# Optimization experiments

Measured on AMD Instinct MI355X. Metric: run time of the kernel, lower is better.

Reference implementation:

```python
import jax, jax.numpy as jnp
import numpy as np

V_TH = 1.0

def spike_fn(x):
    # Heaviside spike (surrogate gradient only matters for bwd)
    return (x > 0).astype(x.dtype)

def setup_inputs() -> dict:
    key = jax.random.key(0)
    ks = jax.random.split(key, 7)
    B, T, I = 256, 512, 512
    H, NB, O = 1024, 4, 128
    HB = H // NB
    x = jax.random.normal(ks[0], (B, T, I), dtype=jnp.float32)
    v0 = jax.random.uniform(ks[1], (B, H), dtype=jnp.float32)  # torch.rand init
    W_branch = jax.random.normal(ks[2], (NB, I, HB), dtype=jnp.float32) * (1.0 / np.sqrt(I))
    tau_n = jax.random.uniform(ks[3], (NB, HB), minval=2.0, maxval=6.0, dtype=jnp.float32)
    tau_m = jax.random.uniform(ks[4], (H,), minval=0.0, maxval=4.0, dtype=jnp.float32)
    W_out = jax.random.normal(ks[5], (H, O), dtype=jnp.float32) * (1.0 / np.sqrt(H))
    b_out = jnp.zeros((O,), dtype=jnp.float32)
    return {"x": x, "v0": v0, "W_branch": W_branch, "tau_n": tau_n,
            "tau_m": tau_m, "W_out": W_out, "b_out": b_out}

def reference(x, v0, W_branch, tau_n, tau_m, W_out, b_out):
    B, T, I = x.shape
    NB, _, HB = W_branch.shape
    H = NB * HB
    beta = jax.nn.sigmoid(tau_n)[:, None, :]   # (NB, 1, HB)
    alpha = jax.nn.sigmoid(tau_m)              # (H,)
    xt = jnp.transpose(x, (1, 0, 2))           # (T, B, I)
    mask = (jnp.arange(T) >= T // 2).astype(x.dtype)  # integrate 2nd half only

    def step(carry, inp):
        d, v, s, acc = carry
        x_t, m = inp
        branch_in = jnp.einsum('bi,nio->nbo', x_t, W_branch)  # (NB, B, HB)
        d = beta * d + (1.0 - beta) * branch_in
        total = jnp.transpose(d, (1, 0, 2)).reshape(B, H)      # cat branches dim=1
        v = alpha * v + (1.0 - alpha) * total - V_TH * s
        s = spike_fn(v - V_TH)
        acc = acc + s * m
        return (d, v, s, acc), None

    d0 = jnp.zeros((NB, B, HB), dtype=x.dtype)
    s0 = jnp.zeros((B, H), dtype=x.dtype)
    acc0 = jnp.zeros((B, H), dtype=x.dtype)
    (d, v, s, acc), _ = jax.lax.scan(step, (d0, v0, s0, acc0), (xt, mask))
    return acc @ W_out + b_out
```

## Files before the change

kernel.cpp:

```cpp
#include <hip/hip_runtime.h>
#include <hip/hip_bf16.h>

#define BSZ 256
#define TT  512
#define II  512
#define HH  1024
#define OO  128
#define BH  262144
#define TC  256

typedef short bfrag8 __attribute__((ext_vector_type(8)));
typedef float f32x4  __attribute__((ext_vector_type(4)));

__device__ __forceinline__ unsigned short f2bf(float f) {
    union { float f; unsigned int u; } c; c.f = f;
    unsigned int u = c.u;
    unsigned int r = u + 0x7fffu + ((u >> 16) & 1u);
    return (unsigned short)(r >> 16);
}
__device__ __forceinline__ float bf2f(unsigned short h) {
    union { unsigned int u; float f; } c; c.u = ((unsigned int)h) << 16;
    return c.f;
}

__device__ __forceinline__ void pack2(float f0, float f1, int& hi, int& lo) {
    __hip_bfloat162 h2 = __float22bfloat162_rn(make_float2(f0, f1));
    float r0 = f0 - __bfloat162float(h2.x);
    float r1 = f1 - __bfloat162float(h2.y);
    __hip_bfloat162 l2 = __float22bfloat162_rn(make_float2(r0, r1));
    union { __hip_bfloat162 b; int i; } ch, cl;
    ch.b = h2; cl.b = l2;
    hi = ch.i; lo = cl.i;
}

__global__ __launch_bounds__(256) void setup_k(const float* __restrict__ Wb,
                                               const float* __restrict__ v0,
                                               unsigned short* __restrict__ Whi,
                                               unsigned short* __restrict__ Wlo,
                                               float* __restrict__ dS, float* __restrict__ vS,
                                               float* __restrict__ sS, float* __restrict__ aS) {
    int idx = blockIdx.x * 256 + threadIdx.x;
    int n = idx >> 17;
    int rem = idx & 131071;
    int i = rem >> 8;
    int o = rem & 255;
    int h = (n << 8) + o;
    float w = Wb[idx];
    unsigned short hi = f2bf(w);
    float fh = bf2f(hi);
    unsigned short lo = f2bf(w - fh);
    Whi[(size_t)h * II + i] = hi;
    Wlo[(size_t)h * II + i] = lo;
    if (idx < BH) {
        dS[idx] = 0.0f; vS[idx] = v0[idx]; sS[idx] = 0.0f; aS[idx] = 0.0f;
    }
}

__global__ __launch_bounds__(256) void split_x(const float* __restrict__ X,
    unsigned short* __restrict__ Xhi, unsigned short* __restrict__ Xlo)
{
    size_t idx = ((size_t)blockIdx.x * 256 + threadIdx.x) << 3;
    f32x4 v0 = *(const f32x4*)(X + idx);
    f32x4 v1 = *(const f32x4*)(X + idx + 4);
    union { uint4 v; int i[4]; } H, L;
    pack2(v0.x, v0.y, H.i[0], L.i[0]);
    pack2(v0.z, v0.w, H.i[1], L.i[1]);
    pack2(v1.x, v1.y, H.i[2], L.i[2]);
    pack2(v1.z, v1.w, H.i[3], L.i[3]);
    *(uint4*)(Xhi + idx) = H.v;
    *(uint4*)(Xlo + idx) = L.v;
}

#define GLL16(G, Lp) __builtin_amdgcn_global_load_lds(                         \
    (const __attribute__((address_space(1))) void*)(G),                        \
    (__attribute__((address_space(3))) void*)(Lp), 16, 0, 0)

#define BAR() do { asm volatile("" ::: "memory");                              \
                   __builtin_amdgcn_s_barrier();                               \
                   asm volatile("" ::: "memory"); } while (0)

#define STAGE(K0, BUFB) do {                                                   \
    _Pragma("unroll") for (int j_ = 0; j_ < 4; ++j_) {                         \
        int w8_ = (j_ << 3) + wv;                                              \
        GLL16(gA + (K0) + ((size_t)w8_ << 12), smem + (BUFB) + (w8_ << 10));   \
        GLL16(gB + (K0) + ((size_t)w8_ << 12), smem + (BUFB) + 32768 + (w8_ << 10)); \
    } } while (0)

#define LDA2(F, BUFB, H0, L0, H1, L1) do {                                     \
    const char* p_ = smem + (BUFB) + aRow + ((F) << 11);                       \
    H0 = *(const bfrag8*)(p_ + sH);                                            \
    L0 = *(const bfrag8*)(p_ + sL);                                            \
    H1 = *(const bfrag8*)(p_ + 2048 + sH);                                     \
    L1 = *(const bfrag8*)(p_ + 2048 + sL);                                     \
} while (0)

#define LOADB(BUFB) do {                                                       \
    const char* p_ = smem + (BUFB) + bRow;                                     \
    _Pragma("unroll") for (int g_ = 0; g_ < 4; ++g_) {                         \
        bh[g_] = *(const bfrag8*)(p_ + (g_ << 11) + sH);                       \
        bl[g_] = *(const bfrag8*)(p_ + (g_ << 11) + sL);                       \
    } } while (0)

#define MFMA3(AH, AL, BHG, BLG, C) do {                                        \
    C = __builtin_amdgcn_mfma_f32_16x16x32_bf16(AH, BHG, C, 0, 0, 0);          \
    C = __builtin_amdgcn_mfma_f32_16x16x32_bf16(AH, BLG, C, 0, 0, 0);          \
    C = __builtin_amdgcn_mfma_f32_16x16x32_bf16(AL, BHG, C, 0, 0, 0);          \
} while (0)

#define MM2(F, H0, L0, H1, L1) do {                                            \
    __builtin_amdgcn_s_setprio(1);                                             \
    _Pragma("unroll") for (int g_ = 0; g_ < 4; ++g_) {                         \
        MFMA3(H0, L0, bh[g_], bl[g_], acc[F][g_]);                             \
        MFMA3(H1, L1, bh[g_], bl[g_], acc[(F) + 1][g_]);                       \
    }                                                                          \
    __builtin_amdgcn_s_setprio(0);                                             \
} while (0)

__global__ __launch_bounds__(512, 2) void gemm8(
    const unsigned short* __restrict__ Xhi, const unsigned short* __restrict__ Xlo,
    const unsigned short* __restrict__ Whi, const unsigned short* __restrict__ Wlo,
    float* __restrict__ U, int xrow0)
{
    extern __shared__ char smem[];

    const int P = blockIdx.x;
    const int L = ((P & 7) << 7) | (P >> 3);
    const int m0 = (L >> 2) << 8;
    const int h0 = (L & 3) << 8;

    const int tid = threadIdx.x;
    const int lane = tid & 63;
    const int wv = tid >> 6;
    const int l16 = lane & 15;
    const int q = lane >> 4;
    const int wm = wv >> 2, wn = wv & 3;

    const int e = l16 & 7;
    const int sH = ((q ^ e) << 4);
    const int sL = (((q + 4) ^ e) << 4);
    const int aRow = ((wm << 7) + l16) << 7;
    const int bRow = (((wn << 6) + l16) << 7) + 32768;

    const int rl = lane >> 3;
    const int sp = (lane & 7) ^ rl;
    const int grow0 = (m0 << 1) + xrow0;
    const unsigned short* gA = (sp < 4)
        ? (Xhi + ((size_t)(grow0 + rl) << 9) + (sp << 3))
        : (Xlo + ((size_t)(grow0 + rl) << 9) + ((sp - 4) << 3));
    const unsigned short* gB = (sp < 4)
        ? (Whi + ((size_t)(h0 + rl) << 9) + (sp << 3))
        : (Wlo + ((size_t)(h0 + rl) << 9) + ((sp - 4) << 3));

    f32x4 acc[8][4];
#pragma unroll
    for (int i = 0; i < 8; ++i)
#pragma unroll
        for (int j = 0; j < 4; ++j)
#pragma unroll
            for (int r = 0; r < 4; ++r) acc[i][j][r] = 0.0f;

    bfrag8 a0h, a0l, a1h, a1l;
    bfrag8 b0h, b0l, b1h, b1l;
    bfrag8 bh[4], bl[4];

    STAGE(0, 0);
    STAGE(32, 65536);
    asm volatile("s_waitcnt vmcnt(8)" ::: "memory");
    __builtin_amdgcn_s_barrier();
    asm volatile("" ::: "memory");
    LDA2(0, 0, a0h, a0l, a1h, a1l);

#pragma unroll 1
    for (int tt = 0; tt < 16; tt += 2) {
        const int k2 = (tt << 5) + 64;
        LOADB(0);
        LDA2(2, 0, b0h, b0l, b1h, b1l);
        MM2(0, a0h, a0l, a1h, a1l);
        BAR();
        LDA2(4, 0, a0h, a0l, a1h, a1l);
        MM2(2, b0h, b0l, b1h, b1l);
        BAR();
        LDA2(6, 0, b0h, b0l, b1h, b1l);
        MM2(4, a0h, a0l, a1h, a1l);
        asm volatile("s_waitcnt lgkmcnt(0)" ::: "memory");
        BAR();
        if (tt < 14) {
            STAGE(k2, 0);
            MM2(6, b0h, b0l, b1h, b1l);
            asm volatile("s_waitcnt vmcnt(8)" ::: "memory");
        } else {
            MM2(6, b0h, b0l, b1h, b1l);
            asm volatile("s_waitcnt vmcnt(0)" ::: "memory");
        }
        LDA2(0, 65536, a0h, a0l, a1h, a1l);
        BAR();
        LOADB(65536);
        LDA2(2, 65536, b0h, b0l, b1h, b1l);
        MM2(0, a0h, a0l, a1h, a1l);
        BAR();
        LDA2(4, 65536, a0h, a0l, a1h, a1l);
        MM2(2, b0h, b0l, b1h, b1l);
        BAR();
        LDA2(6, 65536, b0h, b0l, b1h, b1l);
        MM2(4, a0h, a0l, a1h, a1l);
        asm volatile("s_waitcnt lgkmcnt(0)" ::: "memory");
        BAR();
        if (tt < 13) {
            STAGE(k2 + 32, 65536);
            MM2(6, b0h, b0l, b1h, b1l);
            asm volatile("s_waitcnt vmcnt(8)" ::: "memory");
            LDA2(0, 0, a0h, a0l, a1h, a1l);
        } else {
            MM2(6, b0h, b0l, b1h, b1l);
        }
        BAR();
    }

#pragma unroll
    for (int f = 0; f < 8; ++f) {
        const int rb = m0 + (wm << 7) + (f << 4) + (q << 2);
#pragma unroll
        for (int rr = 0; rr < 4; ++rr) {
            const int m = rb + rr;
            const size_t base =
                (((size_t)((m & 255) << 8) + (m >> 8)) << 10) + h0 + (wn << 6) + l16;
#pragma unroll
            for (int g = 0; g < 4; ++g) U[base + (g << 4)] = acc[f][g][rr];
        }
    }
}

__global__ __launch_bounds__(256) void scan_chunk(const float* __restrict__ U,
    const float* __restrict__ tau_n, const float* __restrict__ tau_m,
    float* __restrict__ dS, float* __restrict__ vS,
    float* __restrict__ sS, float* __restrict__ aS, int t0, int Tc)
{
    int idx = blockIdx.x * 256 + threadIdx.x;
    int h = idx & (HH - 1);
    float beta  = 1.0f / (1.0f + __expf(-tau_n[h]));
    float alpha = 1.0f / (1.0f + __expf(-tau_m[h]));
    float ob = 1.0f - beta, oa = 1.0f - alpha;
    float dd = dS[idx], vv = vS[idx], ss = sS[idx], aa = aS[idx];
    const float* Up = U + idx;

    float u[16];
#pragma unroll
    for (int j = 0; j < 16; ++j) u[j] = Up[(size_t)j << 18];

    int tg = 0;
    for (; tg + 16 < Tc; tg += 16) {
#pragma unroll
        for (int j = 0; j < 16; ++j) {
            float uu = u[j];
            u[j] = Up[(size_t)(tg + 16 + j) << 18];
            float msk = ((t0 + tg + j) >= (TT / 2)) ? 1.0f : 0.0f;
            dd = beta * dd + ob * uu;
            vv = alpha * vv + oa * dd - ss;
            ss = (vv > 1.0f) ? 1.0f : 0.0f;
            aa += msk * ss;
        }
    }
#pragma unroll
    for (int j = 0; j < 16; ++j) {
        float uu = u[j];
        float msk = ((t0 + tg + j) >= (TT / 2)) ? 1.0f : 0.0f;
        dd = beta * dd + ob * uu;
        vv = alpha * vv + oa * dd - ss;
        ss = (vv > 1.0f) ? 1.0f : 0.0f;
        aa += msk * ss;
    }
    dS[idx] = dd; vS[idx] = vv; sS[idx] = ss; aS[idx] = aa;
}

__global__ __launch_bounds__(256) void out_gemm(const float* __restrict__ acc,
    const float* __restrict__ Wout, const float* __restrict__ bout,
    float* __restrict__ out)
{
    __shared__ float a_s[HH];
    __shared__ float partial[OO];
    int b = blockIdx.x;
    int o = threadIdx.x & (OO - 1);
    int half = threadIdx.x >> 7;
    for (int i = threadIdx.x; i < HH; i += 256) a_s[i] = acc[b * HH + i];
    __syncthreads();
    float sum = half ? 0.0f : bout[o];
    const float* Wp = Wout + (size_t)half * 512 * OO + o;
    const float* ap = a_s + half * 512;
#pragma unroll 8
    for (int h = 0; h < 512; ++h) sum = fmaf(ap[h], Wp[(size_t)h * OO], sum);
    if (half) partial[o] = sum;
    __syncthreads();
    if (!half) out[b * OO + o] = sum + partial[o];
}

extern "C" void kernel_launch(void* const* d_in, const int* in_sizes, int n_in,
                              void* d_out, int out_size, void* d_ws, size_t ws_size,
                              hipStream_t stream) {
    const float* x     = (const float*)d_in[0];
    const float* v0    = (const float*)d_in[1];
    const float* Wb    = (const float*)d_in[2];
    const float* tau_n = (const float*)d_in[3];
    const float* tau_m = (const float*)d_in[4];
    const float* Wout  = (const float*)d_in[5];
    const float* bout  = (const float*)d_in[6];
    float* out = (float*)d_out;

    char* ws = (char*)d_ws;
    unsigned short* Whi = (unsigned short*)(ws);
    unsigned short* Wlo = (unsigned short*)(ws + (1ll << 20));
    float* dS = (float*)(ws + (2ll << 20));
    float* vS = (float*)(ws + (3ll << 20));
    float* sS = (float*)(ws + (4ll << 20));
    float* aS = (float*)(ws + (5ll << 20));
    unsigned short* Xhi = (unsigned short*)(ws + (6ll << 20));
    unsigned short* Xlo = (unsigned short*)(ws + (134ll << 20));
    float* U  = (float*)(ws + (262ll << 20));

    hipFuncSetAttribute((const void*)gemm8,
                        hipFuncAttributeMaxDynamicSharedMemorySize, 131072);

    setup_k<<<2048, 256, 0, stream>>>(Wb, v0, Whi, Wlo, dS, vS, sS, aS);
    split_x<<<32768, 256, 0, stream>>>(x, Xhi, Xlo);

    for (int t0 = 0; t0 < TT; t0 += TC) {
        gemm8<<<1024, 512, 131072, stream>>>(Xhi, Xlo, Whi, Wlo, U, t0);
        scan_chunk<<<BH / 256, 256, 0, stream>>>(U, tau_n, tau_m, dS, vS, sS, aS, t0, TC);
    }
    out_gemm<<<BSZ, 256, 0, stream>>>(aS, Wout, bout, out);
}
```

Baseline: 936.9 us.

## Fuse recurrent scan into GEMM epilogue via LDS transpose, drop U buffer

The membrane/dendrite recurrence is now computed inside the GEMM kernel's epilogue. Accumulator tiles are written to shared memory in a swizzled layout, and 256 threads scan the timesteps sequentially per hidden unit. This removes the large global intermediate U and the separate scan kernel launch, trading them for a serialized per-block scan tail. During that tail only half of the threads work, which lengthens each GEMM block.

```diff
diff --git a/kernel.cpp b/kernel.cpp
--- a/kernel.cpp
+++ b/kernel.cpp
@@ -119,7 +119,9 @@
 __global__ __launch_bounds__(512, 2) void gemm8(
     const unsigned short* __restrict__ Xhi, const unsigned short* __restrict__ Xlo,
     const unsigned short* __restrict__ Whi, const unsigned short* __restrict__ Wlo,
-    float* __restrict__ U, int xrow0)
+    const float* __restrict__ tau_n, const float* __restrict__ tau_m,
+    float* __restrict__ dS, float* __restrict__ vS,
+    float* __restrict__ sS, float* __restrict__ aS, int xrow0)
 {
     extern __shared__ char smem[];
 
@@ -127,6 +129,7 @@
     const int L = ((P & 7) << 7) | (P >> 3);
     const int m0 = (L >> 2) << 8;
     const int h0 = (L & 3) << 8;
+    const int b  = L >> 2;
 
     const int tid = threadIdx.x;
     const int lane = tid & 63;
@@ -216,60 +219,51 @@
         BAR();
     }
 
-#pragma unroll
-    for (int f = 0; f < 8; ++f) {
-        const int rb = m0 + (wm << 7) + (f << 4) + (q << 2);
-#pragma unroll
-        for (int rr = 0; rr < 4; ++rr) {
-            const int m = rb + rr;
-            const size_t base =
-                (((size_t)((m & 255) << 8) + (m >> 8)) << 10) + h0 + (wn << 6) + l16;
-#pragma unroll
-            for (int g = 0; g < 4; ++g) U[base + (g << 4)] = acc[f][g][rr];
+    float dd = 0.f, vv = 0.f, ssp = 0.f, aa = 0.f, beta = 0.f, alpha = 0.f, ob = 0.f, oa = 0.f;
+    if (tid < 256) {
+        const int hg = h0 + tid;
+        const int sidx = b * HH + hg;
+        beta  = 1.0f / (1.0f + __expf(-tau_n[hg]));
+        alpha = 1.0f / (1.0f + __expf(-tau_m[hg]));
+        ob = 1.0f - beta; oa = 1.0f - alpha;
+        dd = dS[sidx]; vv = vS[sidx]; ssp = sS[sidx]; aa = aS[sidx];
+    }
+    const float lv = (xrow0 >= TT / 2) ? 1.0f : 0.0f;
+
+#pragma unroll
+    for (int R = 0; R < 2; ++R) {
+        if (wm == R) {
+#pragma unroll
+            for (int f = 0; f < 8; ++f)
+#pragma unroll
+                for (int g = 0; g < 4; ++g) {
+                    const int hloc = (wn << 6) + (g << 4) + l16;
+                    const int slot = (f << 2) + q;
+                    *(f32x4*)(smem + (hloc << 9) + ((slot ^ (hloc & 7)) << 4)) = acc[f][g];
+                }
         }
-    }
-}
-
-__global__ __launch_bounds__(256) void scan_chunk(const float* __restrict__ U,
-    const float* __restrict__ tau_n, const float* __restrict__ tau_m,
-    float* __restrict__ dS, float* __restrict__ vS,
-    float* __restrict__ sS, float* __restrict__ aS, int t0, int Tc)
-{
-    int idx = blockIdx.x * 256 + threadIdx.x;
-    int h = idx & (HH - 1);
-    float beta  = 1.0f / (1.0f + __expf(-tau_n[h]));
-    float alpha = 1.0f / (1.0f + __expf(-tau_m[h]));
-    float ob = 1.0f - beta, oa = 1.0f - alpha;
-    float dd = dS[idx], vv = vS[idx], ss = sS[idx], aa = aS[idx];
-    const float* Up = U + idx;
-
-    float u[16];
-#pragma unroll
-    for (int j = 0; j < 16; ++j) u[j] = Up[(size_t)j << 18];
-
-    int tg = 0;
-    for (; tg + 16 < Tc; tg += 16) {
-#pragma unroll
-        for (int j = 0; j < 16; ++j) {
-            float uu = u[j];
-            u[j] = Up[(size_t)(tg + 16 + j) << 18];
-            float msk = ((t0 + tg + j) >= (TT / 2)) ? 1.0f : 0.0f;
-            dd = beta * dd + ob * uu;
-            vv = alpha * vv + oa * dd - ss;
-            ss = (vv > 1.0f) ? 1.0f : 0.0f;
-            aa += msk * ss;
+        __syncthreads();
+        if (tid < 256) {
+            const char* bp = smem + (tid << 9);
+            const int eh = tid & 7;
+#pragma unroll 8
+            for (int s4 = 0; s4 < 32; ++s4) {
+                f32x4 u4 = *(const f32x4*)(bp + ((s4 ^ eh) << 4));
+#pragma unroll
+                for (int r = 0; r < 4; ++r) {
+                    dd = beta * dd + ob * u4[r];
+                    vv = alpha * vv + oa * dd - ssp;
+                    ssp = (vv > 1.0f) ? 1.0f : 0.0f;
+                    aa += lv * ssp;
+                }
+            }
         }
-    }
-#pragma unroll
-    for (int j = 0; j < 16; ++j) {
-        float uu = u[j];
-        float msk = ((t0 + tg + j) >= (TT / 2)) ? 1.0f : 0.0f;
-        dd = beta * dd + ob * uu;
-        vv = alpha * vv + oa * dd - ss;
-        ss = (vv > 1.0f) ? 1.0f : 0.0f;
-        aa += msk * ss;
-    }
-    dS[idx] = dd; vS[idx] = vv; sS[idx] = ss; aS[idx] = aa;
+        __syncthreads();
+    }
+    if (tid < 256) {
+        const int sidx = b * HH + h0 + tid;
+        dS[sidx] = dd; vS[sidx] = vv; sS[sidx] = ssp; aS[sidx] = aa;
+    }
 }
 
 __global__ __launch_bounds__(256) void out_gemm(const float* __restrict__ acc,
@@ -314,7 +308,6 @@
     float* aS = (float*)(ws + (5ll << 20));
     unsigned short* Xhi = (unsigned short*)(ws + (6ll << 20));
     unsigned short* Xlo = (unsigned short*)(ws + (134ll << 20));
-    float* U  = (float*)(ws + (262ll << 20));
 
     hipFuncSetAttribute((const void*)gemm8,
                         hipFuncAttributeMaxDynamicSharedMemorySize, 131072);
@@ -323,8 +316,8 @@
     split_x<<<32768, 256, 0, stream>>>(x, Xhi, Xlo);
 
     for (int t0 = 0; t0 < TT; t0 += TC) {
-        gemm8<<<1024, 512, 131072, stream>>>(Xhi, Xlo, Whi, Wlo, U, t0);
-        scan_chunk<<<BH / 256, 256, 0, stream>>>(U, tau_n, tau_m, dS, vS, sS, aS, t0, TC);
+        gemm8<<<1024, 512, 131072, stream>>>(Xhi, Xlo, Whi, Wlo, tau_n, tau_m,
+                                             dS, vS, sS, aS, t0);
     }
     out_gemm<<<BSZ, 256, 0, stream>>>(aS, Wout, bout, out);
 }
```

Measured after the change: 818.9 us. -12.6%, faster.
